# Performance work log

Measured on AMD Instinct MI355X. Metric: run time of the kernel, lower is better.

## Reference

```python
import jax, jax.numpy as jnp
import numpy as np

B, S, H, L, V = 128, 512, 1024, 4, 32000


def setup_inputs() -> dict:
    key = jax.random.key(0)
    ks = jax.random.split(key, 7)
    lengths = jax.random.randint(ks[0], (B,), 1, S + 1)
    lengths = lengths.at[0].set(S)  # force max length == S so T is static
    tok = jax.random.randint(ks[1], (B, S), 1, V)  # nonzero tokens inside length
    pos = jnp.arange(S)[None, :]
    x = jnp.where(pos < lengths[:, None], tok, 0)  # 0 = pad (x>0 defines length)
    emb = jax.random.normal(ks[2], (V, H), dtype=jnp.float32) * 0.02
    W_ih = jax.random.normal(ks[3], (L, 4 * H, H), dtype=jnp.float32) / np.float32(np.sqrt(H))
    W_hh = jax.random.normal(ks[4], (L, 4 * H, H), dtype=jnp.float32) / np.float32(np.sqrt(H))
    b_ih = jax.random.normal(ks[5], (L, 4 * H), dtype=jnp.float32) * 0.01
    b_hh = jax.random.normal(ks[6], (L, 4 * H), dtype=jnp.float32) * 0.01
    return {"x": x, "emb": emb, "W_ih": W_ih, "W_hh": W_hh, "b_ih": b_ih, "b_hh": b_hh}


def reference(x, emb, W_ih, W_hh, b_ih, b_hh):
    # lengths and pack's descending sort (pack_padded_sequence, enforce_sorted=False)
    lengths = jnp.sum(x > 0, axis=1)                         # [B]
    sorted_idx = jnp.argsort(-lengths, stable=True)          # sorted (desc) order
    unsort_idx = jnp.argsort(sorted_idx)                     # packed.unsorted_indices

    # Source bug: `start` is never advanced, so every iteration runs a ONE-step
    # stacked LSTM (zero init state) on packed.data[0:bs_t] == t=0 embeddings of
    # the bs_t longest sequences. Compute that single step once on all rows.
    xt = emb[x[sorted_idx, 0]]                               # [B, H] sorted order
    h0 = jnp.zeros_like(xt)                                  # zero initial hidden
    hs, cs = [], []
    for l in range(W_ih.shape[0]):
        gates = xt @ W_ih[l].T + b_ih[l] + h0 @ W_hh[l].T + b_hh[l]
        i, f, g, o = jnp.split(gates, 4, axis=-1)            # torch LSTMCell order
        c = jax.nn.sigmoid(i) * jnp.tanh(g)                  # f * c0 = 0
        h = jax.nn.sigmoid(o) * jnp.tanh(c)
        xt = h
        hs.append(h)
        cs.append(c)

    # output[t, b] = top-layer h for original seq b, zeroed where t >= lengths[b]
    T = x.shape[1]                                           # max length == S
    h_top = xt[unsort_idx]                                   # back to original order
    tmask = (jnp.arange(T)[:, None] < lengths[None, :]).astype(h_top.dtype)  # [T,B]
    output = tmask[:, :, None] * h_top[None, :, :]           # [T, B, H]

    # state from the LAST loop iteration: sorted order, rows >= bs_last zero-padded
    bs_last = jnp.sum(lengths >= T)                          # batch size at t = T-1
    smask = (jnp.arange(x.shape[0]) < bs_last).astype(h_top.dtype)[None, :, None]
    state_h = jnp.stack(hs, axis=0) * smask                  # [L, B, H]
    state_c = jnp.stack(cs, axis=0) * smask                  # [L, B, H]
    return output, state_h, state_c
```

## Files before the change

### kernel.cpp

```cpp
#include <hip/hip_runtime.h>

#define Bn 128
#define Sn 512
#define Hn 1024
#define Ln 4

typedef float nfloat4 __attribute__((ext_vector_type(4)));

__device__ __forceinline__ float sigmoidf_(float x) { return 1.0f / (1.0f + __expf(-x)); }

__global__ __launch_bounds__(128) void len_kernel(const int* __restrict__ x, int* __restrict__ lengths) {
  const int b = blockIdx.x, t = threadIdx.x;
  int4 v = ((const int4*)x)[b * 128 + t];
  int c = (v.x > 0) + (v.y > 0) + (v.z > 0) + (v.w > 0);
  for (int off = 32; off > 0; off >>= 1) c += __shfl_down(c, off);
  __shared__ int tmp[2];
  if ((t & 63) == 0) tmp[t >> 6] = c;
  __syncthreads();
  if (t == 0) lengths[b] = tmp[0] + tmp[1];
}

__global__ __launch_bounds__(128) void sort_kernel(const int* __restrict__ x, const int* __restrict__ lengths,
                                                   int* __restrict__ rank, int* __restrict__ tok_sorted,
                                                   int* __restrict__ bs_last) {
  __shared__ int sl[128];
  __shared__ int cnt;
  const int b = threadIdx.x;
  const int len = lengths[b];
  sl[b] = len;
  if (b == 0) cnt = 0;
  __syncthreads();
  int r = 0;
  for (int b2 = 0; b2 < 128; b2++) {
    int l2 = sl[b2];
    r += (l2 > len) || (l2 == len && b2 < b);
  }
  rank[b] = r;
  tok_sorted[r] = x[b * Sn];
  if (len >= Sn) atomicAdd(&cnt, 1);
  __syncthreads();
  if (b == 0) bs_last[0] = cnt;
}

__global__ __launch_bounds__(256) void gemm_kernel(const float* __restrict__ xt,
                                                   const int* __restrict__ tok,
                                                   const float* __restrict__ Wl,
                                                   float* __restrict__ part) {
  __shared__ float xtT[32][132];
  __shared__ float Ws[32][96];
  __shared__ int sTok[128];
  const int t = threadIdx.x;
  const int mtile = blockIdx.x & 31;
  const int kc = blockIdx.x >> 5;
  const int rg = t & 31;
  const int msub = t >> 5;
  const int k0 = kc * 128;
  const int kv4 = (t & 7) * 4;

  if (tok != nullptr) {
    if (t < 128) sTok[t] = tok[t];
    __syncthreads();
  }
  const float* xrow[4];
#pragma unroll
  for (int i = 0; i < 4; i++) {
    const int r = i * 32 + (t >> 3);
    const int row = (tok != nullptr) ? sTok[r] : r;
    xrow[i] = xt + (size_t)row * 1024;
  }

  float acc[3][4][4];
#pragma unroll
  for (int q = 0; q < 3; q++)
#pragma unroll
    for (int mm = 0; mm < 4; mm++)
#pragma unroll
      for (int rr = 0; rr < 4; rr++) acc[q][mm][rr] = 0.0f;

  float4 xreg[4], wreg[3];
  {
#pragma unroll
    for (int i = 0; i < 4; i++) xreg[i] = *(const float4*)&xrow[i][k0 + kv4];
#pragma unroll
    for (int i = 0; i < 3; i++) {
      int jj = i * 32 + (t >> 3);
      int q = jj >> 5, mloc = jj & 31;
      int qoff = (q == 0) ? 0 : ((q == 1) ? 2048 : 3072);
      wreg[i] = *(const float4*)&Wl[(size_t)(qoff + mtile * 32 + mloc) * 1024 + k0 + kv4];
    }
  }

#pragma unroll
  for (int tile = 0; tile < 4; tile++) {
    __syncthreads();
#pragma unroll
    for (int i = 0; i < 4; i++) {
      const int r = i * 32 + (t >> 3);
      xtT[kv4 + 0][r] = xreg[i].x;
      xtT[kv4 + 1][r] = xreg[i].y;
      xtT[kv4 + 2][r] = xreg[i].z;
      xtT[kv4 + 3][r] = xreg[i].w;
    }
#pragma unroll
    for (int i = 0; i < 3; i++) {
      const int jj = i * 32 + (t >> 3);
      Ws[kv4 + 0][jj] = wreg[i].x;
      Ws[kv4 + 1][jj] = wreg[i].y;
      Ws[kv4 + 2][jj] = wreg[i].z;
      Ws[kv4 + 3][jj] = wreg[i].w;
    }
    float4 xnxt[4], wnxt[3];
    if (tile < 3) {
      const int kt = k0 + (tile + 1) * 32;
#pragma unroll
      for (int i = 0; i < 4; i++) xnxt[i] = *(const float4*)&xrow[i][kt + kv4];
#pragma unroll
      for (int i = 0; i < 3; i++) {
        int jj = i * 32 + (t >> 3);
        int q = jj >> 5, mloc = jj & 31;
        int qoff = (q == 0) ? 0 : ((q == 1) ? 2048 : 3072);
        wnxt[i] = *(const float4*)&Wl[(size_t)(qoff + mtile * 32 + mloc) * 1024 + kt + kv4];
      }
    }
    __syncthreads();
#pragma unroll
    for (int kk = 0; kk < 32; kk++) {
      const float4 xv = *(const float4*)&xtT[kk][rg * 4];
      const float4 w0 = *(const float4*)&Ws[kk][msub * 4];
      const float4 w1 = *(const float4*)&Ws[kk][32 + msub * 4];
      const float4 w2 = *(const float4*)&Ws[kk][64 + msub * 4];
      const float xa[4] = {xv.x, xv.y, xv.z, xv.w};
      const float wv[3][4] = {{w0.x, w0.y, w0.z, w0.w},
                              {w1.x, w1.y, w1.z, w1.w},
                              {w2.x, w2.y, w2.z, w2.w}};
#pragma unroll
      for (int q = 0; q < 3; q++)
#pragma unroll
        for (int mm = 0; mm < 4; mm++)
#pragma unroll
          for (int rr = 0; rr < 4; rr++)
            acc[q][mm][rr] = fmaf(wv[q][mm], xa[rr], acc[q][mm][rr]);
    }
    if (tile < 3) {
#pragma unroll
      for (int i = 0; i < 4; i++) xreg[i] = xnxt[i];
#pragma unroll
      for (int i = 0; i < 3; i++) wreg[i] = wnxt[i];
    }
  }

  const int mbase = mtile * 32 + msub * 4;
#pragma unroll
  for (int q = 0; q < 3; q++)
#pragma unroll
    for (int mm = 0; mm < 4; mm++) {
      float4 v = make_float4(acc[q][mm][0], acc[q][mm][1], acc[q][mm][2], acc[q][mm][3]);
      *(float4*)&part[(((size_t)kc * 3 + q) * 1024 + (mbase + mm)) * 128 + rg * 4] = v;
    }
}

__global__ __launch_bounds__(256) void act_kernel(const float* __restrict__ part,
                                                  const float* __restrict__ bih,
                                                  const float* __restrict__ bhh,
                                                  const int* __restrict__ bs_last,
                                                  float* __restrict__ xt_out,
                                                  float* __restrict__ sh,
                                                  float* __restrict__ sc) {
  __shared__ float red[128][12];
  const int t = threadIdx.x;
  const int r = t & 127;
  const int half = t >> 7;
  const int m0 = blockIdx.x * 4;
  float s[3][4];
#pragma unroll
  for (int q = 0; q < 3; q++)
#pragma unroll
    for (int mm = 0; mm < 4; mm++) s[q][mm] = 0.0f;
#pragma unroll
  for (int k4 = 0; k4 < 4; k4++) {
    const int kcc = half * 4 + k4;
#pragma unroll
    for (int q = 0; q < 3; q++)
#pragma unroll
      for (int mm = 0; mm < 4; mm++)
        s[q][mm] += part[(((size_t)kcc * 3 + q) * 1024 + (m0 + mm)) * 128 + r];
  }
  if (half == 1) {
#pragma unroll
    for (int q = 0; q < 3; q++)
#pragma unroll
      for (int mm = 0; mm < 4; mm++) red[r][q * 4 + mm] = s[q][mm];
  }
  __syncthreads();
  if (half == 0) {
    const int bs = bs_last[0];
    float hv[4], cv[4];
#pragma unroll
    for (int mm = 0; mm < 4; mm++) {
      const int m = m0 + mm;
      const float si = s[0][mm] + red[r][0 * 4 + mm] + bih[m] + bhh[m];
      const float sg = s[1][mm] + red[r][1 * 4 + mm] + bih[2048 + m] + bhh[2048 + m];
      const float so = s[2][mm] + red[r][2 * 4 + mm] + bih[3072 + m] + bhh[3072 + m];
      const float c = sigmoidf_(si) * tanhf(sg);
      const float h = sigmoidf_(so) * tanhf(c);
      hv[mm] = h;
      cv[mm] = c;
    }
    const float msk = (r < bs) ? 1.0f : 0.0f;
    *(float4*)&xt_out[(size_t)r * 1024 + m0] = make_float4(hv[0], hv[1], hv[2], hv[3]);
    *(float4*)&sh[(size_t)r * 1024 + m0] =
        make_float4(msk * hv[0], msk * hv[1], msk * hv[2], msk * hv[3]);
    *(float4*)&sc[(size_t)r * 1024 + m0] =
        make_float4(msk * cv[0], msk * cv[1], msk * cv[2], msk * cv[3]);
  }
}

__global__ __launch_bounds__(256) void bcast_kernel(const float* __restrict__ hfin,
                                                    const int* __restrict__ lengths,
                                                    const int* __restrict__ rank,
                                                    float* __restrict__ out) {
  const int b = blockIdx.x & 127;
  const int c = blockIdx.x >> 7;
  const int len = lengths[b];
  const int t0 = c * 64;
  nfloat4 v = (nfloat4)0.0f;
  if (t0 < len) v = ((const nfloat4*)hfin)[rank[b] * 256 + threadIdx.x];
  int valid = len - t0;
  valid = valid < 0 ? 0 : (valid > 64 ? 64 : valid);
  nfloat4* p = (nfloat4*)out + ((size_t)t0 * 128 + b) * 256 + threadIdx.x;
  for (int i = 0; i < valid; i++) {
    __builtin_nontemporal_store(v, p);
    p += 32768;
  }
  const nfloat4 z = (nfloat4)0.0f;
  for (int i = valid; i < 64; i++) {
    __builtin_nontemporal_store(z, p);
    p += 32768;
  }
}

extern "C" void kernel_launch(void* const* d_in, const int* in_sizes, int n_in,
                              void* d_out, int out_size, void* d_ws, size_t ws_size,
                              hipStream_t stream) {
  const int* x = (const int*)d_in[0];
  const float* emb = (const float*)d_in[1];
  const float* W_ih = (const float*)d_in[2];
  const float* b_ih = (const float*)d_in[4];
  const float* b_hh = (const float*)d_in[5];

  float* out = (float*)d_out;
  float* sh = out + (size_t)Sn * Bn * Hn;
  float* sc = sh + (size_t)Ln * Bn * Hn;
  float* part = out;

  char* ws = (char*)d_ws;
  int* lengths = (int*)ws;
  int* rank = lengths + 128;
  int* tok_sorted = rank + 128;
  int* bs_last = tok_sorted + 128;
  float* xtA = (float*)(ws + 4096);
  float* xtB = xtA + 128 * 1024;

  len_kernel<<<128, 128, 0, stream>>>(x, lengths);
  sort_kernel<<<1, 128, 0, stream>>>(x, lengths, rank, tok_sorted, bs_last);

  float* bufs[2] = {xtA, xtB};
  const float* xin = emb;
  const int* tokp = tok_sorted;
  for (int l = 0; l < Ln; l++) {
    gemm_kernel<<<256, 256, 0, stream>>>(xin, tokp, W_ih + (size_t)l * 4 * Hn * Hn, part);
    act_kernel<<<256, 256, 0, stream>>>(part, b_ih + l * 4 * Hn, b_hh + l * 4 * Hn, bs_last,
                                        bufs[l & 1], sh + (size_t)l * Bn * Hn,
                                        sc + (size_t)l * Bn * Hn);
    xin = bufs[l & 1];
    tokp = nullptr;
  }
  bcast_kernel<<<1024, 256, 0, stream>>>(xin, lengths, rank, out);
}
```

Measured before the change: 495.1 us.

## Replace FP32 SIMT GEMM with split-bf16 MFMA GEMM using three-product emulation

Replaces the FP32 FMA GEMM with a bf16 MFMA kernel. Each operand is split into hi and lo bf16 parts and three MFMA products (hh, hl, lh) are summed to approximate FP32 accuracy. A new gather kernel converts the embedding rows to split bf16, and the activation kernel now writes split bf16 copies of h for the next layer, using the output buffer as scratch. K chunks are enlarged so there are fewer partial sums to reduce, and W is converted in each block from FP32. The cost is slightly reduced precision and extra conversion work.

Result: faster. 475.9 us (-3.9%).

```diff
diff --git a/kernel.cpp b/kernel.cpp
--- a/kernel.cpp
+++ b/kernel.cpp
@@ -6,8 +6,19 @@
 #define Ln 4
 
 typedef float nfloat4 __attribute__((ext_vector_type(4)));
+typedef __attribute__((ext_vector_type(8))) short short8;
+typedef __attribute__((ext_vector_type(4))) float f32x4;
 
 __device__ __forceinline__ float sigmoidf_(float x) { return 1.0f / (1.0f + __expf(-x)); }
+
+__device__ __forceinline__ unsigned short bf16hi(float f) {
+  unsigned u = __float_as_uint(f);
+  u = u + 0x7FFFu + ((u >> 16) & 1u);
+  return (unsigned short)(u >> 16);
+}
+__device__ __forceinline__ float bf16tof(unsigned short h) {
+  return __uint_as_float(((unsigned)h) << 16);
+}
 
 __global__ __launch_bounds__(128) void len_kernel(const int* __restrict__ x, int* __restrict__ lengths) {
   const int b = blockIdx.x, t = threadIdx.x;
@@ -42,120 +53,102 @@
   if (b == 0) bs_last[0] = cnt;
 }
 
-__global__ __launch_bounds__(256) void gemm_kernel(const float* __restrict__ xt,
-                                                   const int* __restrict__ tok,
-                                                   const float* __restrict__ Wl,
-                                                   float* __restrict__ part) {
-  __shared__ float xtT[32][132];
-  __shared__ float Ws[32][96];
-  __shared__ int sTok[128];
+__global__ __launch_bounds__(256) void gather_cvt(const int* __restrict__ tok_sorted,
+                                                  const float* __restrict__ emb,
+                                                  unsigned short* __restrict__ xhi,
+                                                  unsigned short* __restrict__ xlo) {
+  const int r = blockIdx.x, t = threadIdx.x;
+  const int tok = tok_sorted[r];
+  float4 v = ((const float4*)emb)[(size_t)tok * 256 + t];
+  float f[4] = {v.x, v.y, v.z, v.w};
+  unsigned short hh[4], ll[4];
+#pragma unroll
+  for (int j = 0; j < 4; j++) {
+    hh[j] = bf16hi(f[j]);
+    ll[j] = bf16hi(f[j] - bf16tof(hh[j]));
+  }
+  ((ushort4*)xhi)[r * 256 + t] = make_ushort4(hh[0], hh[1], hh[2], hh[3]);
+  ((ushort4*)xlo)[r * 256 + t] = make_ushort4(ll[0], ll[1], ll[2], ll[3]);
+}
+
+__global__ __launch_bounds__(256) void gemm_mfma(const unsigned short* __restrict__ xhi,
+                                                 const unsigned short* __restrict__ xlo,
+                                                 const float* __restrict__ Wl,
+                                                 float* __restrict__ part) {
+  __shared__ unsigned short Whi[64][264];
+  __shared__ unsigned short Wlo[64][264];
   const int t = threadIdx.x;
-  const int mtile = blockIdx.x & 31;
-  const int kc = blockIdx.x >> 5;
-  const int rg = t & 31;
-  const int msub = t >> 5;
-  const int k0 = kc * 128;
-  const int kv4 = (t & 7) * 4;
-
-  if (tok != nullptr) {
-    if (t < 128) sTok[t] = tok[t];
-    __syncthreads();
-  }
-  const float* xrow[4];
-#pragma unroll
-  for (int i = 0; i < 4; i++) {
-    const int r = i * 32 + (t >> 3);
-    const int row = (tok != nullptr) ? sTok[r] : r;
-    xrow[i] = xt + (size_t)row * 1024;
-  }
-
-  float acc[3][4][4];
-#pragma unroll
-  for (int q = 0; q < 3; q++)
-#pragma unroll
-    for (int mm = 0; mm < 4; mm++)
-#pragma unroll
-      for (int rr = 0; rr < 4; rr++) acc[q][mm][rr] = 0.0f;
-
-  float4 xreg[4], wreg[3];
-  {
-#pragma unroll
-    for (int i = 0; i < 4; i++) xreg[i] = *(const float4*)&xrow[i][k0 + kv4];
-#pragma unroll
-    for (int i = 0; i < 3; i++) {
-      int jj = i * 32 + (t >> 3);
-      int q = jj >> 5, mloc = jj & 31;
-      int qoff = (q == 0) ? 0 : ((q == 1) ? 2048 : 3072);
-      wreg[i] = *(const float4*)&Wl[(size_t)(qoff + mtile * 32 + mloc) * 1024 + k0 + kv4];
-    }
-  }
-
-#pragma unroll
-  for (int tile = 0; tile < 4; tile++) {
-    __syncthreads();
-#pragma unroll
-    for (int i = 0; i < 4; i++) {
-      const int r = i * 32 + (t >> 3);
-      xtT[kv4 + 0][r] = xreg[i].x;
-      xtT[kv4 + 1][r] = xreg[i].y;
-      xtT[kv4 + 2][r] = xreg[i].z;
-      xtT[kv4 + 3][r] = xreg[i].w;
-    }
-#pragma unroll
-    for (int i = 0; i < 3; i++) {
-      const int jj = i * 32 + (t >> 3);
-      Ws[kv4 + 0][jj] = wreg[i].x;
-      Ws[kv4 + 1][jj] = wreg[i].y;
-      Ws[kv4 + 2][jj] = wreg[i].z;
-      Ws[kv4 + 3][jj] = wreg[i].w;
-    }
-    float4 xnxt[4], wnxt[3];
-    if (tile < 3) {
-      const int kt = k0 + (tile + 1) * 32;
-#pragma unroll
-      for (int i = 0; i < 4; i++) xnxt[i] = *(const float4*)&xrow[i][kt + kv4];
-#pragma unroll
-      for (int i = 0; i < 3; i++) {
-        int jj = i * 32 + (t >> 3);
-        int q = jj >> 5, mloc = jj & 31;
-        int qoff = (q == 0) ? 0 : ((q == 1) ? 2048 : 3072);
-        wnxt[i] = *(const float4*)&Wl[(size_t)(qoff + mtile * 32 + mloc) * 1024 + kt + kv4];
+  const int bid = blockIdx.x;
+  const int nt = bid % 48;
+  const int kc = bid / 48;
+  const int q = nt >> 4;
+  const int qoff = (q == 0) ? 0 : ((q == 1) ? 2048 : 3072);
+  const int mrow0 = qoff + (nt & 15) * 64;
+  const int k0 = kc * 256;
+
+#pragma unroll
+  for (int i = 0; i < 16; i++) {
+    const int vi = i * 256 + t;
+    const int c = vi >> 6;
+    const int ks4 = (vi & 63) * 4;
+    float4 w4 = *(const float4*)&Wl[(size_t)(mrow0 + c) * 1024 + k0 + ks4];
+    float f[4] = {w4.x, w4.y, w4.z, w4.w};
+    unsigned short hh[4], ll[4];
+#pragma unroll
+    for (int j = 0; j < 4; j++) {
+      hh[j] = bf16hi(f[j]);
+      ll[j] = bf16hi(f[j] - bf16tof(hh[j]));
+    }
+    *(ushort4*)&Whi[c][ks4] = make_ushort4(hh[0], hh[1], hh[2], hh[3]);
+    *(ushort4*)&Wlo[c][ks4] = make_ushort4(ll[0], ll[1], ll[2], ll[3]);
+  }
+  __syncthreads();
+
+  const int w = t >> 6;
+  const int l = t & 63;
+  const int lrow = l & 15;
+  const int lk8 = (l >> 4) * 8;
+
+  f32x4 acc[2][4];
+#pragma unroll
+  for (int rt = 0; rt < 2; rt++)
+#pragma unroll
+    for (int ct = 0; ct < 4; ct++) acc[rt][ct] = (f32x4)0.0f;
+
+  const unsigned short* xh0 = xhi + (size_t)(w * 32 + lrow) * 1024 + k0 + lk8;
+  const unsigned short* xl0 = xlo + (size_t)(w * 32 + lrow) * 1024 + k0 + lk8;
+
+#pragma unroll
+  for (int ks = 0; ks < 8; ks++) {
+    const int kk = ks * 32;
+    short8 ah[2], al[2], bh[4], bl[4];
+#pragma unroll
+    for (int rt = 0; rt < 2; rt++) {
+      ah[rt] = *(const short8*)(xh0 + rt * 16 * 1024 + kk);
+      al[rt] = *(const short8*)(xl0 + rt * 16 * 1024 + kk);
+    }
+#pragma unroll
+    for (int ct = 0; ct < 4; ct++) {
+      bh[ct] = *(const short8*)&Whi[ct * 16 + lrow][kk + lk8];
+      bl[ct] = *(const short8*)&Wlo[ct * 16 + lrow][kk + lk8];
+    }
+#pragma unroll
+    for (int rt = 0; rt < 2; rt++)
+#pragma unroll
+      for (int ct = 0; ct < 4; ct++) {
+        acc[rt][ct] = __builtin_amdgcn_mfma_f32_16x16x32_bf16(ah[rt], bh[ct], acc[rt][ct], 0, 0, 0);
+        acc[rt][ct] = __builtin_amdgcn_mfma_f32_16x16x32_bf16(ah[rt], bl[ct], acc[rt][ct], 0, 0, 0);
+        acc[rt][ct] = __builtin_amdgcn_mfma_f32_16x16x32_bf16(al[rt], bh[ct], acc[rt][ct], 0, 0, 0);
       }
-    }
-    __syncthreads();
-#pragma unroll
-    for (int kk = 0; kk < 32; kk++) {
-      const float4 xv = *(const float4*)&xtT[kk][rg * 4];
-      const float4 w0 = *(const float4*)&Ws[kk][msub * 4];
-      const float4 w1 = *(const float4*)&Ws[kk][32 + msub * 4];
-      const float4 w2 = *(const float4*)&Ws[kk][64 + msub * 4];
-      const float xa[4] = {xv.x, xv.y, xv.z, xv.w};
-      const float wv[3][4] = {{w0.x, w0.y, w0.z, w0.w},
-                              {w1.x, w1.y, w1.z, w1.w},
-                              {w2.x, w2.y, w2.z, w2.w}};
-#pragma unroll
-      for (int q = 0; q < 3; q++)
-#pragma unroll
-        for (int mm = 0; mm < 4; mm++)
-#pragma unroll
-          for (int rr = 0; rr < 4; rr++)
-            acc[q][mm][rr] = fmaf(wv[q][mm], xa[rr], acc[q][mm][rr]);
-    }
-    if (tile < 3) {
-#pragma unroll
-      for (int i = 0; i < 4; i++) xreg[i] = xnxt[i];
-#pragma unroll
-      for (int i = 0; i < 3; i++) wreg[i] = wnxt[i];
-    }
-  }
-
-  const int mbase = mtile * 32 + msub * 4;
-#pragma unroll
-  for (int q = 0; q < 3; q++)
-#pragma unroll
-    for (int mm = 0; mm < 4; mm++) {
-      float4 v = make_float4(acc[q][mm][0], acc[q][mm][1], acc[q][mm][2], acc[q][mm][3]);
-      *(float4*)&part[(((size_t)kc * 3 + q) * 1024 + (mbase + mm)) * 128 + rg * 4] = v;
+  }
+
+  const int rbase = w * 32 + (l >> 4) * 4;
+#pragma unroll
+  for (int rt = 0; rt < 2; rt++)
+#pragma unroll
+    for (int ct = 0; ct < 4; ct++) {
+      const int m = (nt & 15) * 64 + ct * 16 + lrow;
+      *(f32x4*)&part[(((size_t)kc * 3 + q) * 1024 + m) * 128 + rbase + rt * 16] = acc[rt][ct];
     }
 }
 
@@ -165,7 +158,9 @@
                                                   const int* __restrict__ bs_last,
                                                   float* __restrict__ xt_out,
                                                   float* __restrict__ sh,
-                                                  float* __restrict__ sc) {
+                                                  float* __restrict__ sc,
+                                                  unsigned short* __restrict__ xhi_out,
+                                                  unsigned short* __restrict__ xlo_out) {
   __shared__ float red[128][12];
   const int t = threadIdx.x;
   const int r = t & 127;
@@ -173,28 +168,29 @@
   const int m0 = blockIdx.x * 4;
   float s[3][4];
 #pragma unroll
-  for (int q = 0; q < 3; q++)
-#pragma unroll
-    for (int mm = 0; mm < 4; mm++) s[q][mm] = 0.0f;
-#pragma unroll
-  for (int k4 = 0; k4 < 4; k4++) {
-    const int kcc = half * 4 + k4;
-#pragma unroll
-    for (int q = 0; q < 3; q++)
+  for (int qq = 0; qq < 3; qq++)
+#pragma unroll
+    for (int mm = 0; mm < 4; mm++) s[qq][mm] = 0.0f;
+#pragma unroll
+  for (int k2 = 0; k2 < 2; k2++) {
+    const int kcc = half * 2 + k2;
+#pragma unroll
+    for (int qq = 0; qq < 3; qq++)
 #pragma unroll
       for (int mm = 0; mm < 4; mm++)
-        s[q][mm] += part[(((size_t)kcc * 3 + q) * 1024 + (m0 + mm)) * 128 + r];
+        s[qq][mm] += part[(((size_t)kcc * 3 + qq) * 1024 + (m0 + mm)) * 128 + r];
   }
   if (half == 1) {
 #pragma unroll
-    for (int q = 0; q < 3; q++)
-#pragma unroll
-      for (int mm = 0; mm < 4; mm++) red[r][q * 4 + mm] = s[q][mm];
+    for (int qq = 0; qq < 3; qq++)
+#pragma unroll
+      for (int mm = 0; mm < 4; mm++) red[r][qq * 4 + mm] = s[qq][mm];
   }
   __syncthreads();
   if (half == 0) {
     const int bs = bs_last[0];
     float hv[4], cv[4];
+    unsigned short hh[4], ll[4];
 #pragma unroll
     for (int mm = 0; mm < 4; mm++) {
       const int m = m0 + mm;
@@ -205,6 +201,8 @@
       const float h = sigmoidf_(so) * tanhf(c);
       hv[mm] = h;
       cv[mm] = c;
+      hh[mm] = bf16hi(h);
+      ll[mm] = bf16hi(h - bf16tof(hh[mm]));
     }
     const float msk = (r < bs) ? 1.0f : 0.0f;
     *(float4*)&xt_out[(size_t)r * 1024 + m0] = make_float4(hv[0], hv[1], hv[2], hv[3]);
@@ -212,6 +210,8 @@
         make_float4(msk * hv[0], msk * hv[1], msk * hv[2], msk * hv[3]);
     *(float4*)&sc[(size_t)r * 1024 + m0] =
         make_float4(msk * cv[0], msk * cv[1], msk * cv[2], msk * cv[3]);
+    *(ushort4*)&xhi_out[(size_t)r * 1024 + m0] = make_ushort4(hh[0], hh[1], hh[2], hh[3]);
+    *(ushort4*)&xlo_out[(size_t)r * 1024 + m0] = make_ushort4(ll[0], ll[1], ll[2], ll[3]);
   }
 }
 
@@ -252,6 +252,11 @@
   float* sh = out + (size_t)Sn * Bn * Hn;
   float* sc = sh + (size_t)Ln * Bn * Hn;
   float* part = out;
+  unsigned short* bfbase = (unsigned short*)(out + (size_t)2097152);
+  unsigned short* xhiA = bfbase;
+  unsigned short* xloA = bfbase + 131072;
+  unsigned short* xhiB = bfbase + 262144;
+  unsigned short* xloB = bfbase + 393216;
 
   char* ws = (char*)d_ws;
   int* lengths = (int*)ws;
@@ -263,17 +268,19 @@
 
   len_kernel<<<128, 128, 0, stream>>>(x, lengths);
   sort_kernel<<<1, 128, 0, stream>>>(x, lengths, rank, tok_sorted, bs_last);
-
-  float* bufs[2] = {xtA, xtB};
-  const float* xin = emb;
-  const int* tokp = tok_sorted;
+  gather_cvt<<<128, 256, 0, stream>>>(tok_sorted, emb, xhiA, xloA);
+
+  float* xtF[2] = {xtA, xtB};
+  unsigned short* hiP[2] = {xhiA, xhiB};
+  unsigned short* loP[2] = {xloA, xloB};
+  int cur = 0;
   for (int l = 0; l < Ln; l++) {
-    gemm_kernel<<<256, 256, 0, stream>>>(xin, tokp, W_ih + (size_t)l * 4 * Hn * Hn, part);
+    const int nxt = cur ^ 1;
+    gemm_mfma<<<192, 256, 0, stream>>>(hiP[cur], loP[cur], W_ih + (size_t)l * 4 * Hn * Hn, part);
     act_kernel<<<256, 256, 0, stream>>>(part, b_ih + l * 4 * Hn, b_hh + l * 4 * Hn, bs_last,
-                                        bufs[l & 1], sh + (size_t)l * Bn * Hn,
-                                        sc + (size_t)l * Bn * Hn);
-    xin = bufs[l & 1];
-    tokp = nullptr;
-  }
-  bcast_kernel<<<1024, 256, 0, stream>>>(xin, lengths, rank, out);
-}
+                                        xtF[l & 1], sh + (size_t)l * Bn * Hn,
+                                        sc + (size_t)l * Bn * Hn, hiP[nxt], loP[nxt]);
+    cur = nxt;
+  }
+  bcast_kernel<<<1024, 256, 0, stream>>>(xtF[1], lengths, rank, out);
+}
```
